# Kernel optimization log

Measured on AMD Instinct MI355X. Metric: run time of the kernel, lower is better.

Reference implementation:

```python
import jax, jax.numpy as jnp
import numpy as np

VOCAB = 32000
D_MODEL = 192
N_LAYERS = 8
D_STATE = 64
EXPAND = 2
D_CONV = 3
NUM_CLASSES = 2
D_INNER = EXPAND * D_MODEL            # 384
DT_RANK = (D_MODEL + 15) // 16        # 12 (mamba_ssm default ceil(d_model/16))
EPS = 1e-6


def rmsnorm(x, w):
    return w * x * jax.lax.rsqrt(jnp.mean(x * x, axis=-1, keepdims=True) + EPS)


def selective_scan(u, dt, A, Bm, Cm):
    # u, dt: (b, T, d_inner); Bm, Cm: (b, T, d_state); A: (d_inner, d_state)
    def step(h, xs):
        dt_t, B_t, C_t, u_t = xs                      # (b,di),(b,ds),(b,ds),(b,di)
        dA = jnp.exp(dt_t[:, :, None] * A)            # (b, di, ds)
        h = dA * h + (dt_t * u_t)[:, :, None] * B_t[:, None, :]
        y = jnp.einsum('bdn,bn->bd', h, C_t)
        return h, y

    b = u.shape[0]
    h0 = jnp.zeros((b, D_INNER, D_STATE), u.dtype)
    xs = (jnp.swapaxes(dt, 0, 1), jnp.swapaxes(Bm, 0, 1),
          jnp.swapaxes(Cm, 0, 1), jnp.swapaxes(u, 0, 1))
    _, ys = jax.lax.scan(step, h0, xs)                # ys: (T, b, di)
    return jnp.swapaxes(ys, 0, 1)


def mamba_layer(x, p):
    # one residual Mamba block: x + Mamba(RMSNorm(x))
    norm_w, in_w, cw, cb, xpw, dtw, dtb, Alog, Dp, ow = p
    h = rmsnorm(x, norm_w)
    xz = jnp.einsum('btd,ed->bte', h, in_w)           # (b, T, 2*di)
    xi, z = jnp.split(xz, 2, axis=-1)
    # causal depthwise conv over time
    xc = jnp.swapaxes(xi, 1, 2)                       # (b, di, T)
    xc = jax.lax.conv_general_dilated(xc, cw[:, None, :], (1,),
                                      [(D_CONV - 1, 0)],
                                      feature_group_count=D_INNER)
    xi = jax.nn.silu(jnp.swapaxes(xc, 1, 2) + cb)
    dbl = jnp.einsum('btc,ec->bte', xi, xpw)          # (b, T, dt_rank+2*ds)
    dt_r = dbl[..., :DT_RANK]
    Bm = dbl[..., DT_RANK:DT_RANK + D_STATE]
    Cm = dbl[..., DT_RANK + D_STATE:]
    dt = jax.nn.softplus(jnp.einsum('btr,dr->btd', dt_r, dtw) + dtb)
    A = -jnp.exp(Alog)
    y = selective_scan(xi, dt, A, Bm, Cm) + xi * Dp
    y = y * jax.nn.silu(z)
    return x + jnp.einsum('bte,de->btd', y, ow)


def setup_inputs():
    key = jax.random.key(0)
    ks = jax.random.split(key, 12)
    B, L = 8, 1024
    s = 0.02
    input_ids = jax.random.randint(ks[0], (B, L), 0, VOCAB, dtype=jnp.int32)
    attention_mask = jnp.ones((B, L), dtype=jnp.int32)
    embed = jax.random.normal(ks[1], (VOCAB, D_MODEL), jnp.float32) * s
    cls = jax.random.normal(ks[2], (1, 1, D_MODEL), jnp.float32) * s
    norm_w = jnp.ones((N_LAYERS, D_MODEL), jnp.float32)
    in_proj_w = jax.random.normal(ks[3], (N_LAYERS, 2 * D_INNER, D_MODEL), jnp.float32) * s
    conv_w = jax.random.normal(ks[4], (N_LAYERS, D_INNER, D_CONV), jnp.float32) * s
    conv_b = jnp.zeros((N_LAYERS, D_INNER), jnp.float32)
    x_proj_w = jax.random.normal(ks[5], (N_LAYERS, DT_RANK + 2 * D_STATE, D_INNER), jnp.float32) * s
    dt_proj_w = jax.random.normal(ks[6], (N_LAYERS, D_INNER, DT_RANK), jnp.float32) * s
    dt_proj_b = jnp.zeros((N_LAYERS, D_INNER), jnp.float32)
    # mamba_ssm S4D-real init: A_log = log(1..d_state)
    A_log = jnp.log(jnp.tile(jnp.arange(1.0, D_STATE + 1, dtype=jnp.float32)[None, None, :],
                             (N_LAYERS, D_INNER, 1)))
    D_param = jnp.ones((N_LAYERS, D_INNER), jnp.float32)
    out_proj_w = jax.random.normal(ks[7], (N_LAYERS, D_MODEL, D_INNER), jnp.float32) * s
    final_norm_w = jnp.ones((D_MODEL,), jnp.float32)
    head_w = embed[:NUM_CLASSES]            # tie_embeddings=True
    head_b = jnp.zeros((NUM_CLASSES,), jnp.float32)
    return dict(input_ids=input_ids, attention_mask=attention_mask, embed=embed,
                cls=cls, norm_w=norm_w, in_proj_w=in_proj_w, conv_w=conv_w,
                conv_b=conv_b, x_proj_w=x_proj_w, dt_proj_w=dt_proj_w,
                dt_proj_b=dt_proj_b, A_log=A_log, D_param=D_param,
                out_proj_w=out_proj_w, final_norm_w=final_norm_w,
                head_w=head_w, head_b=head_b)


def reference(input_ids, attention_mask, embed, cls, norm_w, in_proj_w, conv_w,
              conv_b, x_proj_w, dt_proj_w, dt_proj_b, A_log, D_param,
              out_proj_w, final_norm_w, head_w, head_b):
    x = embed[input_ids]                               # (b, L, d)
    b = x.shape[0]
    x = jnp.concatenate([x, jnp.broadcast_to(cls, (b, 1, D_MODEL))], axis=1)
    layer_fn = jax.checkpoint(mamba_layer)

    def body(x, p):
        return layer_fn(x, p), None

    x, _ = jax.lax.scan(body, x, (norm_w, in_proj_w, conv_w, conv_b, x_proj_w,
                                  dt_proj_w, dt_proj_b, A_log, D_param, out_proj_w))
    x = rmsnorm(x, final_norm_w)
    m = attention_mask.astype(x.dtype)                 # (b, L)
    denom = jnp.clip(jnp.sum(m, axis=1, keepdims=True), 1.0, None)
    pooled = jnp.sum(x[:, :-1] * m[..., None], axis=1) / denom
    return pooled @ head_w.T + head_b                  # (b, num_classes)
```

## Files before the change

### kernel.cpp

```cpp
#include <hip/hip_runtime.h>
#include <hip/hip_bf16.h>
#include <cstddef>

namespace {

constexpr int NB   = 8;
constexpr int LSEQ = 1025;
constexpr int TSEQ = 1024;
constexpr int DM   = 192;
constexpr int DI   = 384;
constexpr int DXZ  = 768;
constexpr int DBLW = 140;
constexpr int DTR  = 12;
constexpr int NST  = 64;
constexpr int MROWS = NB * LSEQ;
constexpr int NCH  = 64;
constexpr int CS   = 16;
constexpr int NCH1 = NCH - 1;
constexpr int NDG  = DI / 64;
constexpr int HST  = 32;
constexpr int XPAD = 144;
constexpr float LOG2E = 1.4426950408889634f;

using bf16x8 = __attribute__((ext_vector_type(8))) short;
using f32x4  = __attribute__((ext_vector_type(4))) float;

__device__ __forceinline__ float waveReduceSum(float v) {
#pragma unroll
  for (int o = 32; o; o >>= 1) v += __shfl_xor(v, o, 64);
  return v;
}

__device__ __forceinline__ unsigned short f2bf(float v) {
  __hip_bfloat16 b = __float2bfloat16(v);
  return *reinterpret_cast<unsigned short*>(&b);
}
__device__ __forceinline__ float bf2f(unsigned short u) {
  return __uint_as_float(((unsigned)u) << 16);
}
__device__ __forceinline__ unsigned addpair_bf(unsigned a, unsigned b) {
  float alo = __uint_as_float(a << 16), ahi = __uint_as_float(a & 0xffff0000u);
  float blo = __uint_as_float(b << 16), bhi = __uint_as_float(b & 0xffff0000u);
  return ((unsigned)f2bf(alo + blo)) | (((unsigned)f2bf(ahi + bhi)) << 16);
}

__global__ void embed_kernel(const int* __restrict__ ids, const float* __restrict__ emb,
                             const float* __restrict__ cls, float* __restrict__ x) {
  int idx = blockIdx.x * blockDim.x + threadIdx.x;
  if (idx >= NB * LSEQ * DM) return;
  int d = idx % DM;
  int bt = idx / DM;
  int t = bt % LSEQ, b = bt / LSEQ;
  float v;
  if (t < TSEQ) v = emb[(size_t)ids[b * TSEQ + t] * DM + d];
  else          v = cls[d];
  x[idx] = v;
}

__global__ void cvt_bf16_kernel(const float* __restrict__ src, unsigned short* __restrict__ dst,
                                int n) {
  int idx = blockIdx.x * blockDim.x + threadIdx.x;
  if (idx < n) dst[idx] = f2bf(src[idx]);
}

__global__ void pad_xp_kernel(const float* __restrict__ src, unsigned short* __restrict__ dst) {
  int idx = blockIdx.x * blockDim.x + threadIdx.x;
  if (idx >= 8 * XPAD * DI) return;
  int k = idx % DI;
  int n = (idx / DI) % XPAD;
  int l = idx / (DI * XPAD);
  float v = (n < DBLW) ? src[((size_t)l * DBLW + n) * DI + k] : 0.f;
  dst[idx] = f2bf(v);
}

__global__ void transpose_batched(const float* __restrict__ in, float* __restrict__ out,
                                  int rows, int cols) {
  __shared__ float tile[32][33];
  int l = blockIdx.z;
  int r0 = blockIdx.y * 32, c0 = blockIdx.x * 32;
  const float* src = in + (size_t)l * rows * cols;
  float* dst = out + (size_t)l * rows * cols;
  int tx = threadIdx.x, ty = threadIdx.y;
#pragma unroll
  for (int i = 0; i < 32; i += 8) {
    int r = r0 + ty + i, c = c0 + tx;
    if (r < rows && c < cols) tile[ty + i][tx] = src[(size_t)r * cols + c];
  }
  __syncthreads();
#pragma unroll
  for (int i = 0; i < 32; i += 8) {
    int c = c0 + ty + i, r = r0 + tx;
    if (c < cols && r < rows) dst[(size_t)c * rows + r] = tile[tx][ty + i];
  }
}

__global__ __launch_bounds__(192)
void rmsnorm_kernel(const float* __restrict__ x, const float* __restrict__ w,
                    unsigned short* __restrict__ h) {
  int row = blockIdx.x;
  int d = threadIdx.x;
  float v = x[(size_t)row * DM + d];
  float ss = waveReduceSum(v * v);
  __shared__ float red[3];
  if ((d & 63) == 0) red[d >> 6] = ss;
  __syncthreads();
  float ms = (red[0] + red[1] + red[2]) * (1.f / DM);
  h[(size_t)row * DM + d] = f2bf(v * rsqrtf(ms + 1e-6f) * w[d]);
}

template <int EPI, int ASRC>
__global__ __launch_bounds__(256)
void gemm_mfma(const unsigned short* __restrict__ A, const unsigned short* __restrict__ Ab0,
               const unsigned short* __restrict__ Ab1, const unsigned short* __restrict__ W,
               float* __restrict__ C, unsigned short* __restrict__ Cb,
               int M, int Nw, int Nstore, int K, int ldc) {
  __shared__ unsigned short Alds[128][40];
  __shared__ unsigned short Wlds[64][40];
  const int tid = threadIdx.x;
  const int w = tid >> 6, lane = tid & 63;
  const int r16 = lane & 15, g = lane >> 4;
  const int row0 = blockIdx.y * 128, col0 = blockIdx.x * 64;

  f32x4 acc[2][4];
#pragma unroll
  for (int mi = 0; mi < 2; ++mi)
#pragma unroll
    for (int ni = 0; ni < 4; ++ni) acc[mi][ni] = (f32x4){0.f, 0.f, 0.f, 0.f};

  for (int k0 = 0; k0 < K; k0 += 32) {
#pragma unroll
    for (int cc = 0; cc < 2; ++cc) {
      int c = tid + cc * 256;
      int r = c >> 2, q = c & 3;
      uint4 v = make_uint4(0, 0, 0, 0);
      int grow = row0 + r;
      if (grow < M) {
        if (ASRC == 0) {
          v = *(const uint4*)(A + (size_t)grow * K + k0 + q * 8);
        } else {
          uint4 a = *(const uint4*)(Ab0 + (size_t)grow * K + k0 + q * 8);
          uint4 b = *(const uint4*)(Ab1 + (size_t)grow * K + k0 + q * 8);
          v.x = addpair_bf(a.x, b.x);
          v.y = addpair_bf(a.y, b.y);
          v.z = addpair_bf(a.z, b.z);
          v.w = addpair_bf(a.w, b.w);
        }
      }
      *(uint4*)&Alds[r][q * 8] = v;
    }
    {
      int r = tid >> 2, q = tid & 3;
      uint4 v = make_uint4(0, 0, 0, 0);
      int gn = col0 + r;
      if (gn < Nw) v = *(const uint4*)(W + (size_t)gn * K + k0 + q * 8);
      *(uint4*)&Wlds[r][q * 8] = v;
    }
    __syncthreads();
    bf16x8 a_f[2], b_f[4];
#pragma unroll
    for (int mi = 0; mi < 2; ++mi)
      a_f[mi] = *(const bf16x8*)&Alds[w * 32 + mi * 16 + r16][g * 8];
#pragma unroll
    for (int ni = 0; ni < 4; ++ni)
      b_f[ni] = *(const bf16x8*)&Wlds[ni * 16 + r16][g * 8];
#pragma unroll
    for (int mi = 0; mi < 2; ++mi)
#pragma unroll
      for (int ni = 0; ni < 4; ++ni)
        acc[mi][ni] = __builtin_amdgcn_mfma_f32_16x16x32_bf16(a_f[mi], b_f[ni],
                                                              acc[mi][ni], 0, 0, 0);
    __syncthreads();
  }
#pragma unroll
  for (int mi = 0; mi < 2; ++mi) {
#pragma unroll
    for (int reg = 0; reg < 4; ++reg) {
      int row = row0 + w * 32 + mi * 16 + g * 4 + reg;
      if (row >= M) continue;
#pragma unroll
      for (int ni = 0; ni < 4; ++ni) {
        int col = col0 + ni * 16 + r16;
        if (col >= Nstore) continue;
        size_t idx = (size_t)row * ldc + col;
        if (EPI == 1)      C[idx] += acc[mi][ni][reg];
        else if (EPI == 0) C[idx] = acc[mi][ni][reg];
        else               Cb[idx] = f2bf(acc[mi][ni][reg]);
      }
    }
  }
}

__global__ void conv_kernel(const unsigned short* __restrict__ xz16, const float* __restrict__ cw,
                            const float* __restrict__ cb,
                            unsigned short* __restrict__ xi16,
                            unsigned short* __restrict__ zg16) {
  int idx = blockIdx.x * blockDim.x + threadIdx.x;
  if (idx >= NB * LSEQ * DI) return;
  int c = idx % DI;
  int bt = idx / DI;
  int t = bt % LSEQ, b = bt / LSEQ;
  const unsigned short* src = xz16 + (size_t)b * LSEQ * DXZ + c;
  float s = cb[c];
  float w0 = cw[c * 3 + 0], w1 = cw[c * 3 + 1], w2 = cw[c * 3 + 2];
  if (t >= 2) s = fmaf(w0, bf2f(src[(size_t)(t - 2) * DXZ]), s);
  if (t >= 1) s = fmaf(w1, bf2f(src[(size_t)(t - 1) * DXZ]), s);
  s = fmaf(w2, bf2f(src[(size_t)t * DXZ]), s);
  float sig = 1.f / (1.f + __expf(-s));
  float u = s * sig;
  xi16[idx] = f2bf(u);
  float zv = bf2f(src[(size_t)t * DXZ + DI]);
  float zsig = 1.f / (1.f + __expf(-zv));
  zg16[idx] = f2bf(zv * zsig);
}

__global__ __launch_bounds__(384)
void dt_kernel(const float* __restrict__ dbl, const float* __restrict__ dtwT,
               const float* __restrict__ dtb, float* __restrict__ dtout) {
  int row0 = blockIdx.x * 4;
  int d = threadIdx.x;
  __shared__ float rr[4][DTR];
  if (d < 4 * DTR) rr[d / DTR][d % DTR] = dbl[(size_t)(row0 + d / DTR) * DBLW + (d % DTR)];
  float w[DTR];
#pragma unroll
  for (int r = 0; r < DTR; ++r) w[r] = dtwT[r * DI + d];
  float bias = dtb[d];
  __syncthreads();
#pragma unroll
  for (int q = 0; q < 4; ++q) {
    float s = bias;
#pragma unroll
    for (int r = 0; r < DTR; ++r) s = fmaf(rr[q][r], w[r], s);
    float sp = fmaxf(s, 0.f) + log1pf(__expf(-fabsf(s)));
    dtout[(size_t)(row0 + q) * DI + d] = sp;
  }
}


__global__ __launch_bounds__(768, 6)
void scan_pass1(const float* __restrict__ dtp_, const unsigned short* __restrict__ xi16,
                const float* __restrict__ dbl, const float* __restrict__ Alog,
                float* __restrict__ cumdt, float* __restrict__ H) {
  __shared__ float Bt[CS][64];
  const int tid = threadIdx.x;
  const int w = tid >> 6, lane = tid & 63;
  const int dgrp = w >> 1, half = w & 1;
  const int b = blockIdx.x / NCH1;
  const int c = blockIdx.x % NCH1;
  const int bg = b * NDG + dgrp;
  const int d = dgrp * 64 + lane;
  const int n0 = half * HST;
  const int t0 = c * CS;

  {
    const float* srcB = dbl + ((size_t)b * LSEQ + t0) * DBLW + DTR + lane;
    for (int r = w; r < CS; r += 12) Bt[r][lane] = srcB[(size_t)r * DBLW];
  }

  const float* Ap = Alog + (size_t)d * NST;
  float a0 = __expf(Ap[0]);
  bool okl = true;
#pragma unroll
  for (int j = 0; j < HST; ++j) {
    float aj = __expf(Ap[n0 + j]);
    okl = okl && (fabsf(aj - (float)(n0 + j + 1) * a0) <= 1e-3f * (float)(n0 + j + 1) * fabsf(a0));
  }
  const bool fast = __all(okl);
  const float al2u = -a0 * LOG2E;

  float h[HST];
#pragma unroll
  for (int j = 0; j < HST; ++j) h[j] = 0.f;

  __syncthreads();

  const float* dtp = dtp_ + ((size_t)b * LSEQ + t0) * DI + d;
  const unsigned short* up = xi16 + ((size_t)b * LSEQ + t0) * DI + d;
  float cum = 0.f;
  float dtv = *dtp, uv = bf2f(*up);

  if (fast) {
    for (int t = 0; t < CS; ++t) {
      float n_dt = 0.f, n_u = 0.f;
      if (t + 1 < CS) {
        dtp += DI; up += DI;
        n_dt = *dtp; n_u = bf2f(*up);
      }
      float dtu = dtv * uv;
      float m = dtv * al2u;
      float r1 = exp2f(m);
      float p = (n0 == 0) ? r1 : exp2f(m * (float)(n0 + 1));
      float r2 = r1 * r1, r4 = r2 * r2;
      float s0 = p, s1 = p * r1, s2 = p * r2, s3 = s2 * r1;
#pragma unroll
      for (int k = 0; k < 8; ++k) {
        float4 B4 = *(const float4*)&Bt[t][n0 + 4 * k];
        h[4 * k + 0] = fmaf(s0, h[4 * k + 0], dtu * B4.x);
        h[4 * k + 1] = fmaf(s1, h[4 * k + 1], dtu * B4.y);
        h[4 * k + 2] = fmaf(s2, h[4 * k + 2], dtu * B4.z);
        h[4 * k + 3] = fmaf(s3, h[4 * k + 3], dtu * B4.w);
        if (k < 7) { s0 *= r4; s1 *= r4; s2 *= r4; s3 *= r4; }
      }
      cum += dtv;
      dtv = n_dt; uv = n_u;
    }
  } else {
    for (int t = 0; t < CS; ++t) {
      float n_dt = 0.f, n_u = 0.f;
      if (t + 1 < CS) {
        dtp += DI; up += DI;
        n_dt = *dtp; n_u = bf2f(*up);
      }
      float dtu = dtv * uv;
      for (int j = 0; j < HST; ++j) {
        float aj = -__expf(Ap[n0 + j]) * LOG2E;
        h[j] = fmaf(exp2f(dtv * aj), h[j], dtu * Bt[t][n0 + j]);
      }
      cum += dtv;
      dtv = n_dt; uv = n_u;
    }
  }

  if (half == 0)
    cumdt[(size_t)bg * NCH1 * 64 + (size_t)c * 64 + lane] = cum;
  float* hp = H + ((size_t)bg * NCH + (c + 1)) * NST * 64 + (size_t)n0 * 64 + lane;
#pragma unroll
  for (int j = 0; j < HST; ++j) hp[j * 64] = h[j];
}

__global__ __launch_bounds__(256)
void scan_pass2(const float* __restrict__ cumdt, const float* __restrict__ Alog,
                float* __restrict__ H) {
  int gw = blockIdx.x * 4 + (threadIdx.x >> 6);
  int lane = threadIdx.x & 63;
  int bg = gw >> 4;
  int nq = (gw & 15) * 4;
  int dgrp = bg % NDG;
  int d = dgrp * 64 + lane;

  float al2[4];
#pragma unroll
  for (int j = 0; j < 4; ++j) al2[j] = -__expf(Alog[(size_t)d * NST + nq + j]) * LOG2E;

  float h[4] = {0.f, 0.f, 0.f, 0.f};

  float* H0 = H + ((size_t)bg * NCH) * NST * 64 + (size_t)nq * 64 + lane;
#pragma unroll
  for (int j = 0; j < 4; ++j) H0[j * 64] = 0.f;

  for (int c = 1; c < NCH; ++c) {
    float cum = cumdt[(size_t)bg * NCH1 * 64 + (size_t)(c - 1) * 64 + lane];
    float* Hc = H + ((size_t)bg * NCH + c) * NST * 64 + (size_t)nq * 64 + lane;
#pragma unroll
    for (int j = 0; j < 4; ++j) {
      float he = Hc[j * 64];
      h[j] = fmaf(exp2f(al2[j] * cum), h[j], he);
      Hc[j * 64] = h[j];
    }
  }
}

__global__ __launch_bounds__(768, 6)
void scan_pass3(const float* __restrict__ dtp_, const unsigned short* __restrict__ xi16,
                const unsigned short* __restrict__ zg16, const float* __restrict__ dbl,
                const float* __restrict__ Alog, const float* __restrict__ Dpar,
                const float* __restrict__ H, unsigned short* __restrict__ yb0,
                unsigned short* __restrict__ yb1) {
  __shared__ float Bt[CS + 1][64];
  __shared__ float Ct[CS + 1][64];
  const int tid = threadIdx.x;
  const int w = tid >> 6, lane = tid & 63;
  const int dgrp = w >> 1, half = w & 1;
  const int b = blockIdx.x >> 6;
  const int c = blockIdx.x & 63;
  const int bg = b * NDG + dgrp;
  const int d = dgrp * 64 + lane;
  const int n0 = half * HST;
  const int t0 = c * CS;
  const int nsteps = (c == NCH - 1) ? (LSEQ - t0) : CS;

  {
    if (w < 6) {
      const float* srcB = dbl + ((size_t)b * LSEQ + t0) * DBLW + DTR + lane;
      for (int r = w; r < nsteps; r += 6) Bt[r][lane] = srcB[(size_t)r * DBLW];
    } else {
      const float* srcC = dbl + ((size_t)b * LSEQ + t0) * DBLW + DTR + NST + lane;
      for (int r = w - 6; r < nsteps; r += 6) Ct[r][lane] = srcC[(size_t)r * DBLW];
    }
  }

  const float* Ap = Alog + (size_t)d * NST;
  float a0 = __expf(Ap[0]);
  bool okl = true;
#pragma unroll
  for (int j = 0; j < HST; ++j) {
    float aj = __expf(Ap[n0 + j]);
    okl = okl && (fabsf(aj - (float)(n0 + j + 1) * a0) <= 1e-3f * (float)(n0 + j + 1) * fabsf(a0));
  }
  const bool fast = __all(okl);
  const float al2u = -a0 * LOG2E;

  float Dp = Dpar[d];
  float h[HST];
  {
    const float* hi = H + ((size_t)bg * NCH + c) * NST * 64 + (size_t)n0 * 64 + lane;
#pragma unroll
    for (int j = 0; j < HST; ++j) h[j] = hi[j * 64];
  }

  __syncthreads();

  const float* dtp = dtp_ + ((size_t)b * LSEQ + t0) * DI + d;
  const unsigned short* up = xi16 + ((size_t)b * LSEQ + t0) * DI + d;
  const unsigned short* gp = zg16 + ((size_t)b * LSEQ + t0) * DI + d;
  unsigned short* yp = (half == 0 ? yb0 : yb1) + ((size_t)b * LSEQ + t0) * DI + d;

  float dtv = *dtp, uv = bf2f(*up), gv = bf2f(*gp);

  if (fast) {
    for (int t = 0; t < nsteps; ++t) {
      float n_dt = 0.f, n_u = 0.f, n_g = 0.f;
      if (t + 1 < nsteps) {
        dtp += DI; up += DI; gp += DI;
        n_dt = *dtp; n_u = bf2f(*up); n_g = bf2f(*gp);
      }
      float dtu = dtv * uv;
      float m = dtv * al2u;
      float r1 = exp2f(m);
      float p = (n0 == 0) ? r1 : exp2f(m * (float)(n0 + 1));
      float r2 = r1 * r1, r4 = r2 * r2;
      float s0 = p, s1 = p * r1, s2 = p * r2, s3 = s2 * r1;
      float y = 0.f;
#pragma unroll
      for (int k = 0; k < 8; ++k) {
        float4 B4 = *(const float4*)&Bt[t][n0 + 4 * k];
        float4 C4 = *(const float4*)&Ct[t][n0 + 4 * k];
        h[4 * k + 0] = fmaf(s0, h[4 * k + 0], dtu * B4.x);
        y = fmaf(h[4 * k + 0], C4.x, y);
        h[4 * k + 1] = fmaf(s1, h[4 * k + 1], dtu * B4.y);
        y = fmaf(h[4 * k + 1], C4.y, y);
        h[4 * k + 2] = fmaf(s2, h[4 * k + 2], dtu * B4.z);
        y = fmaf(h[4 * k + 2], C4.z, y);
        h[4 * k + 3] = fmaf(s3, h[4 * k + 3], dtu * B4.w);
        y = fmaf(h[4 * k + 3], C4.w, y);
        if (k < 7) { s0 *= r4; s1 *= r4; s2 *= r4; s3 *= r4; }
      }
      float outv = (half == 0) ? fmaf(uv, Dp, y) * gv : y * gv;
      *yp = f2bf(outv);
      yp += DI;
      dtv = n_dt; uv = n_u; gv = n_g;
    }
  } else {
    for (int t = 0; t < nsteps; ++t) {
      float n_dt = 0.f, n_u = 0.f, n_g = 0.f;
      if (t + 1 < nsteps) {
        dtp += DI; up += DI; gp += DI;
        n_dt = *dtp; n_u = bf2f(*up); n_g = bf2f(*gp);
      }
      float dtu = dtv * uv;
      float y = 0.f;
      for (int j = 0; j < HST; ++j) {
        float aj = -__expf(Ap[n0 + j]) * LOG2E;
        h[j] = fmaf(exp2f(dtv * aj), h[j], dtu * Bt[t][n0 + j]);
        y = fmaf(h[j], Ct[t][n0 + j], y);
      }
      float outv = (half == 0) ? fmaf(uv, Dp, y) * gv : y * gv;
      *yp = f2bf(outv);
      yp += DI;
      dtv = n_dt; uv = n_u; gv = n_g;
    }
  }
}

__global__ __launch_bounds__(192)
void pool1_kernel(const float* __restrict__ x, const int* __restrict__ mask,
                  const float* __restrict__ fw, float* __restrict__ partial) {
  int b = blockIdx.x >> 6;
  int chunk = blockIdx.x & 63;
  int d = threadIdx.x;
  __shared__ float red[3];
  float w = fw[d];
  float acc = 0.f;
  for (int tt = 0; tt < 16; ++tt) {
    int t = chunk * 16 + tt;
    float v = x[((size_t)b * LSEQ + t) * DM + d];
    float ss = waveReduceSum(v * v);
    if ((d & 63) == 0) red[d >> 6] = ss;
    __syncthreads();
    float ms = (red[0] + red[1] + red[2]) * (1.f / DM);
    float m = (float)mask[b * TSEQ + t];
    acc = fmaf(v * rsqrtf(ms + 1e-6f) * w, m, acc);
    __syncthreads();
  }
  partial[((size_t)b * 64 + chunk) * DM + d] = acc;
}

__global__ __launch_bounds__(192)
void pool2_kernel(const float* __restrict__ partial, const int* __restrict__ mask,
                  const float* __restrict__ hw, const float* __restrict__ hb,
                  float* __restrict__ out) {
  int b = blockIdx.x;
  int d = threadIdx.x;
  float s = 0.f;
  for (int c = 0; c < 64; ++c) s += partial[((size_t)b * 64 + c) * DM + d];
  float den = 0.f;
  for (int t = d; t < TSEQ; t += DM) den += (float)mask[b * TSEQ + t];
  den = waveReduceSum(den);
  __shared__ float dred[3];
  __shared__ float pooled[DM];
  if ((d & 63) == 0) dred[d >> 6] = den;
  __syncthreads();
  float denom = fmaxf(dred[0] + dred[1] + dred[2], 1.f);
  pooled[d] = s / denom;
  __syncthreads();
  if (d < 2) {
    float acc = hb[d];
    for (int k = 0; k < DM; ++k) acc = fmaf(pooled[k], hw[d * DM + k], acc);
    out[b * 2 + d] = acc;
  }
}

}

extern "C" void kernel_launch(void* const* d_in, const int* in_sizes, int n_in,
                              void* d_out, int out_size, void* d_ws, size_t ws_size,
                              hipStream_t stream) {
  const int*   ids    = (const int*)d_in[0];
  const int*   mask   = (const int*)d_in[1];
  const float* embed  = (const float*)d_in[2];
  const float* cls    = (const float*)d_in[3];
  const float* norm_w = (const float*)d_in[4];
  const float* in_w   = (const float*)d_in[5];
  const float* conv_w = (const float*)d_in[6];
  const float* conv_b = (const float*)d_in[7];
  const float* xp_w   = (const float*)d_in[8];
  const float* dtw    = (const float*)d_in[9];
  const float* dtb    = (const float*)d_in[10];
  const float* Alog   = (const float*)d_in[11];
  const float* Dpar   = (const float*)d_in[12];
  const float* ow     = (const float*)d_in[13];
  const float* fnw    = (const float*)d_in[14];
  const float* hw     = (const float*)d_in[15];
  const float* hb     = (const float*)d_in[16];
  float* out = (float*)d_out;

  char* base = (char*)d_ws;
  size_t off = 0;
  auto alloc = [&](size_t bytes) -> void* {
    void* p = base + off;
    off = (off + bytes + 255) & ~(size_t)255;
    return p;
  };

  float* x      = (float*)alloc((size_t)NB * LSEQ * DM * 4);
  unsigned short* h16 = (unsigned short*)alloc((size_t)NB * LSEQ * DM * 2);
  unsigned short* xz16 = (unsigned short*)alloc((size_t)NB * LSEQ * DXZ * 2);
  unsigned short* xi16 = (unsigned short*)alloc((size_t)NB * LSEQ * DI * 2);
  unsigned short* zg16 = (unsigned short*)alloc((size_t)NB * LSEQ * DI * 2);
  float* dblb   = (float*)alloc((size_t)NB * LSEQ * DBLW * 4);
  float* dtbuf  = (float*)alloc((size_t)NB * LSEQ * DI * 4);
  unsigned short* yb0 = (unsigned short*)alloc((size_t)NB * LSEQ * DI * 2);
  unsigned short* yb1 = (unsigned short*)alloc((size_t)NB * LSEQ * DI * 2);
  unsigned short* wb_in = (unsigned short*)alloc((size_t)8 * DXZ * DM * 2);
  unsigned short* wb_xp = (unsigned short*)alloc((size_t)8 * XPAD * DI * 2);
  unsigned short* wb_ow = (unsigned short*)alloc((size_t)8 * DM * DI * 2);
  float* wT_dt  = (float*)alloc((size_t)8 * DTR * DI * 4);
  float* partial = (float*)alloc((size_t)NB * 64 * DM * 4);
  float* cumdt  = (float*)alloc((size_t)NB * NDG * NCH1 * 64 * 4);
  float* Hbuf   = (float*)alloc((size_t)NB * NDG * NCH * NST * 64 * 4);

  cvt_bf16_kernel<<<(8 * DXZ * DM + 255) / 256, 256, 0, stream>>>(in_w, wb_in, 8 * DXZ * DM);
  pad_xp_kernel<<<(8 * XPAD * DI + 255) / 256, 256, 0, stream>>>(xp_w, wb_xp);
  cvt_bf16_kernel<<<(8 * DM * DI + 255) / 256, 256, 0, stream>>>(ow, wb_ow, 8 * DM * DI);
  dim3 tb(32, 8);
  transpose_batched<<<dim3(1, 12, 8), tb, 0, stream>>>(dtw, wT_dt, DI, DTR);

  embed_kernel<<<(NB * LSEQ * DM) / 256, 256, 0, stream>>>(ids, embed, cls, x);

  const int mtiles = (MROWS + 127) / 128;
  for (int l = 0; l < 8; ++l) {
    rmsnorm_kernel<<<MROWS, 192, 0, stream>>>(x, norm_w + l * DM, h16);
    gemm_mfma<2, 0><<<dim3(DXZ / 64, mtiles), 256, 0, stream>>>(
        h16, nullptr, nullptr, wb_in + (size_t)l * DXZ * DM, nullptr, xz16,
        MROWS, DXZ, DXZ, DM, DXZ);
    conv_kernel<<<(NB * LSEQ * DI) / 256, 256, 0, stream>>>(
        xz16, conv_w + l * DI * 3, conv_b + l * DI, xi16, zg16);
    gemm_mfma<0, 0><<<dim3(XPAD / 64 + 1, mtiles), 256, 0, stream>>>(
        xi16, nullptr, nullptr, wb_xp + (size_t)l * XPAD * DI, dblb, nullptr,
        MROWS, XPAD, DBLW, DI, DBLW);
    dt_kernel<<<MROWS / 4, DI, 0, stream>>>(dblb, wT_dt + l * DTR * DI, dtb + l * DI, dtbuf);
    scan_pass1<<<NB * NCH1, 768, 0, stream>>>(
        dtbuf, xi16, dblb, Alog + (size_t)l * DI * NST, cumdt, Hbuf);
    scan_pass2<<<(NB * NDG * 16) / 4, 256, 0, stream>>>(
        cumdt, Alog + (size_t)l * DI * NST, Hbuf);
    scan_pass3<<<NB * NCH, 768, 0, stream>>>(
        dtbuf, xi16, zg16, dblb, Alog + (size_t)l * DI * NST, Dpar + l * DI, Hbuf,
        yb0, yb1);
    gemm_mfma<1, 1><<<dim3(DM / 64, mtiles), 256, 0, stream>>>(
        nullptr, yb0, yb1, wb_ow + (size_t)l * DM * DI, x, nullptr,
        MROWS, DM, DM, DI, DM);
  }

  pool1_kernel<<<NB * 64, 192, 0, stream>>>(x, mask, fnw, partial);
  pool2_kernel<<<NB, 192, 0, stream>>>(partial, mask, hw, hb, out);
}
```

Baseline: 1.391 ms.

## Fuse RMSNorm into in-proj GEMM, halve scan chunks, store chunk states in bf16

Folds the RMSNorm into the input-projection GEMM: each block computes per-row inverse RMS from fp32 x and converts normalized values to bf16 while filling LDS, removing the separate norm kernel and the h16 buffer round trip. The chunked scan now uses 32 chunks of 32 steps instead of 64 of 16, and inter-chunk states are stored as bf16, cutting H traffic while lowering occupancy hints. The scan output dot product is split into four accumulators for ILP. Risks include bf16 precision loss in the carried states, recomputation of the row norms in every column tile, and fewer blocks in the scan passes.

```diff
diff --git a/kernel.cpp b/kernel.cpp
--- a/kernel.cpp
+++ b/kernel.cpp
@@ -14,8 +14,8 @@
 constexpr int DTR  = 12;
 constexpr int NST  = 64;
 constexpr int MROWS = NB * LSEQ;
-constexpr int NCH  = 64;
-constexpr int CS   = 16;
+constexpr int NCH  = 32;
+constexpr int CS   = 32;
 constexpr int NCH1 = NCH - 1;
 constexpr int NDG  = DI / 64;
 constexpr int HST  = 32;
@@ -94,26 +94,103 @@
   }
 }
 
-__global__ __launch_bounds__(192)
-void rmsnorm_kernel(const float* __restrict__ x, const float* __restrict__ w,
-                    unsigned short* __restrict__ h) {
-  int row = blockIdx.x;
-  int d = threadIdx.x;
-  float v = x[(size_t)row * DM + d];
-  float ss = waveReduceSum(v * v);
-  __shared__ float red[3];
-  if ((d & 63) == 0) red[d >> 6] = ss;
+__global__ __launch_bounds__(256)
+void gemm_in_fused(const float* __restrict__ X, const float* __restrict__ normw,
+                   const unsigned short* __restrict__ W, unsigned short* __restrict__ Cb,
+                   int M) {
+  __shared__ unsigned short Alds[128][40];
+  __shared__ unsigned short Wlds[64][40];
+  __shared__ float invr[128];
+  __shared__ float nw[DM];
+  const int tid = threadIdx.x;
+  const int w = tid >> 6, lane = tid & 63;
+  const int r16 = lane & 15, g = lane >> 4;
+  const int row0 = blockIdx.y * 128, col0 = blockIdx.x * 64;
+
+  if (tid < DM) nw[tid] = normw[tid];
+  {
+    int r = tid >> 1, u = tid & 1;
+    int grow = row0 + r;
+    float ss = 0.f;
+    if (grow < M) {
+      const float4* src = (const float4*)(X + (size_t)grow * DM + u * 96);
+#pragma unroll
+      for (int i = 0; i < 24; ++i) {
+        float4 v = src[i];
+        ss += v.x * v.x + v.y * v.y + v.z * v.z + v.w * v.w;
+      }
+    }
+    ss += __shfl_xor(ss, 1, 64);
+    if (u == 0) invr[r] = rsqrtf(ss * (1.f / DM) + 1e-6f);
+  }
   __syncthreads();
-  float ms = (red[0] + red[1] + red[2]) * (1.f / DM);
-  h[(size_t)row * DM + d] = f2bf(v * rsqrtf(ms + 1e-6f) * w[d]);
+
+  f32x4 acc[2][4];
+#pragma unroll
+  for (int mi = 0; mi < 2; ++mi)
+#pragma unroll
+    for (int ni = 0; ni < 4; ++ni) acc[mi][ni] = (f32x4){0.f, 0.f, 0.f, 0.f};
+
+  for (int k0 = 0; k0 < DM; k0 += 32) {
+#pragma unroll
+    for (int cc = 0; cc < 2; ++cc) {
+      int c = tid + cc * 256;
+      int r = c >> 2, q = c & 3;
+      uint4 v = make_uint4(0, 0, 0, 0);
+      int grow = row0 + r;
+      if (grow < M) {
+        const float* s0 = X + (size_t)grow * DM + k0 + q * 8;
+        float4 p0 = *(const float4*)s0, p1 = *(const float4*)(s0 + 4);
+        float ir = invr[r];
+        int kk = k0 + q * 8;
+        v.x = (unsigned)f2bf(p0.x * ir * nw[kk + 0]) | ((unsigned)f2bf(p0.y * ir * nw[kk + 1]) << 16);
+        v.y = (unsigned)f2bf(p0.z * ir * nw[kk + 2]) | ((unsigned)f2bf(p0.w * ir * nw[kk + 3]) << 16);
+        v.z = (unsigned)f2bf(p1.x * ir * nw[kk + 4]) | ((unsigned)f2bf(p1.y * ir * nw[kk + 5]) << 16);
+        v.w = (unsigned)f2bf(p1.z * ir * nw[kk + 6]) | ((unsigned)f2bf(p1.w * ir * nw[kk + 7]) << 16);
+      }
+      *(uint4*)&Alds[r][q * 8] = v;
+    }
+    {
+      int r = tid >> 2, q = tid & 3;
+      uint4 v = *(const uint4*)(W + (size_t)(col0 + r) * DM + k0 + q * 8);
+      *(uint4*)&Wlds[r][q * 8] = v;
+    }
+    __syncthreads();
+    bf16x8 a_f[2], b_f[4];
+#pragma unroll
+    for (int mi = 0; mi < 2; ++mi)
+      a_f[mi] = *(const bf16x8*)&Alds[w * 32 + mi * 16 + r16][g * 8];
+#pragma unroll
+    for (int ni = 0; ni < 4; ++ni)
+      b_f[ni] = *(const bf16x8*)&Wlds[ni * 16 + r16][g * 8];
+#pragma unroll
+    for (int mi = 0; mi < 2; ++mi)
+#pragma unroll
+      for (int ni = 0; ni < 4; ++ni)
+        acc[mi][ni] = __builtin_amdgcn_mfma_f32_16x16x32_bf16(a_f[mi], b_f[ni],
+                                                              acc[mi][ni], 0, 0, 0);
+    __syncthreads();
+  }
+#pragma unroll
+  for (int mi = 0; mi < 2; ++mi) {
+#pragma unroll
+    for (int reg = 0; reg < 4; ++reg) {
+      int row = row0 + w * 32 + mi * 16 + g * 4 + reg;
+      if (row >= M) continue;
+#pragma unroll
+      for (int ni = 0; ni < 4; ++ni) {
+        int col = col0 + ni * 16 + r16;
+        Cb[(size_t)row * DXZ + col] = f2bf(acc[mi][ni][reg]);
+      }
+    }
+  }
 }
 
 template <int EPI, int ASRC>
 __global__ __launch_bounds__(256)
 void gemm_mfma(const unsigned short* __restrict__ A, const unsigned short* __restrict__ Ab0,
                const unsigned short* __restrict__ Ab1, const unsigned short* __restrict__ W,
-               float* __restrict__ C, unsigned short* __restrict__ Cb,
-               int M, int Nw, int Nstore, int K, int ldc) {
+               float* __restrict__ C, int M, int Nw, int Nstore, int K, int ldc) {
   __shared__ unsigned short Alds[128][40];
   __shared__ unsigned short Wlds[64][40];
   const int tid = threadIdx.x;
@@ -182,9 +259,8 @@
         int col = col0 + ni * 16 + r16;
         if (col >= Nstore) continue;
         size_t idx = (size_t)row * ldc + col;
-        if (EPI == 1)      C[idx] += acc[mi][ni][reg];
-        else if (EPI == 0) C[idx] = acc[mi][ni][reg];
-        else               Cb[idx] = f2bf(acc[mi][ni][reg]);
+        if (EPI == 1) C[idx] += acc[mi][ni][reg];
+        else          C[idx] = acc[mi][ni][reg];
       }
     }
   }
@@ -236,10 +312,10 @@
 }
 
 
-__global__ __launch_bounds__(768, 6)
+__global__ __launch_bounds__(768, 3)
 void scan_pass1(const float* __restrict__ dtp_, const unsigned short* __restrict__ xi16,
                 const float* __restrict__ dbl, const float* __restrict__ Alog,
-                float* __restrict__ cumdt, float* __restrict__ H) {
+                float* __restrict__ cumdt, unsigned short* __restrict__ H) {
   __shared__ float Bt[CS][64];
   const int tid = threadIdx.x;
   const int w = tid >> 6, lane = tid & 63;
@@ -322,14 +398,14 @@
 
   if (half == 0)
     cumdt[(size_t)bg * NCH1 * 64 + (size_t)c * 64 + lane] = cum;
-  float* hp = H + ((size_t)bg * NCH + (c + 1)) * NST * 64 + (size_t)n0 * 64 + lane;
-#pragma unroll
-  for (int j = 0; j < HST; ++j) hp[j * 64] = h[j];
+  unsigned short* hp = H + ((size_t)bg * NCH + (c + 1)) * NST * 64 + (size_t)n0 * 64 + lane;
+#pragma unroll
+  for (int j = 0; j < HST; ++j) hp[j * 64] = f2bf(h[j]);
 }
 
 __global__ __launch_bounds__(256)
 void scan_pass2(const float* __restrict__ cumdt, const float* __restrict__ Alog,
-                float* __restrict__ H) {
+                unsigned short* __restrict__ H) {
   int gw = blockIdx.x * 4 + (threadIdx.x >> 6);
   int lane = threadIdx.x & 63;
   int bg = gw >> 4;
@@ -343,35 +419,35 @@
 
   float h[4] = {0.f, 0.f, 0.f, 0.f};
 
-  float* H0 = H + ((size_t)bg * NCH) * NST * 64 + (size_t)nq * 64 + lane;
-#pragma unroll
-  for (int j = 0; j < 4; ++j) H0[j * 64] = 0.f;
+  unsigned short* H0 = H + ((size_t)bg * NCH) * NST * 64 + (size_t)nq * 64 + lane;
+#pragma unroll
+  for (int j = 0; j < 4; ++j) H0[j * 64] = 0;
 
   for (int c = 1; c < NCH; ++c) {
     float cum = cumdt[(size_t)bg * NCH1 * 64 + (size_t)(c - 1) * 64 + lane];
-    float* Hc = H + ((size_t)bg * NCH + c) * NST * 64 + (size_t)nq * 64 + lane;
+    unsigned short* Hc = H + ((size_t)bg * NCH + c) * NST * 64 + (size_t)nq * 64 + lane;
 #pragma unroll
     for (int j = 0; j < 4; ++j) {
-      float he = Hc[j * 64];
+      float he = bf2f(Hc[j * 64]);
       h[j] = fmaf(exp2f(al2[j] * cum), h[j], he);
-      Hc[j * 64] = h[j];
-    }
-  }
-}
-
-__global__ __launch_bounds__(768, 6)
+      Hc[j * 64] = f2bf(h[j]);
+    }
+  }
+}
+
+__global__ __launch_bounds__(768, 3)
 void scan_pass3(const float* __restrict__ dtp_, const unsigned short* __restrict__ xi16,
                 const unsigned short* __restrict__ zg16, const float* __restrict__ dbl,
                 const float* __restrict__ Alog, const float* __restrict__ Dpar,
-                const float* __restrict__ H, unsigned short* __restrict__ yb0,
+                const unsigned short* __restrict__ H, unsigned short* __restrict__ yb0,
                 unsigned short* __restrict__ yb1) {
   __shared__ float Bt[CS + 1][64];
   __shared__ float Ct[CS + 1][64];
   const int tid = threadIdx.x;
   const int w = tid >> 6, lane = tid & 63;
   const int dgrp = w >> 1, half = w & 1;
-  const int b = blockIdx.x >> 6;
-  const int c = blockIdx.x & 63;
+  const int b = blockIdx.x >> 5;
+  const int c = blockIdx.x & 31;
   const int bg = b * NDG + dgrp;
   const int d = dgrp * 64 + lane;
   const int n0 = half * HST;
@@ -402,9 +478,9 @@
   float Dp = Dpar[d];
   float h[HST];
   {
-    const float* hi = H + ((size_t)bg * NCH + c) * NST * 64 + (size_t)n0 * 64 + lane;
-#pragma unroll
-    for (int j = 0; j < HST; ++j) h[j] = hi[j * 64];
+    const unsigned short* hi = H + ((size_t)bg * NCH + c) * NST * 64 + (size_t)n0 * 64 + lane;
+#pragma unroll
+    for (int j = 0; j < HST; ++j) h[j] = bf2f(hi[j * 64]);
   }
 
   __syncthreads();
@@ -429,21 +505,22 @@
       float p = (n0 == 0) ? r1 : exp2f(m * (float)(n0 + 1));
       float r2 = r1 * r1, r4 = r2 * r2;
       float s0 = p, s1 = p * r1, s2 = p * r2, s3 = s2 * r1;
-      float y = 0.f;
+      float y0 = 0.f, y1 = 0.f, y2 = 0.f, y3 = 0.f;
 #pragma unroll
       for (int k = 0; k < 8; ++k) {
         float4 B4 = *(const float4*)&Bt[t][n0 + 4 * k];
         float4 C4 = *(const float4*)&Ct[t][n0 + 4 * k];
         h[4 * k + 0] = fmaf(s0, h[4 * k + 0], dtu * B4.x);
-        y = fmaf(h[4 * k + 0], C4.x, y);
+        y0 = fmaf(h[4 * k + 0], C4.x, y0);
         h[4 * k + 1] = fmaf(s1, h[4 * k + 1], dtu * B4.y);
-        y = fmaf(h[4 * k + 1], C4.y, y);
+        y1 = fmaf(h[4 * k + 1], C4.y, y1);
         h[4 * k + 2] = fmaf(s2, h[4 * k + 2], dtu * B4.z);
-        y = fmaf(h[4 * k + 2], C4.z, y);
+        y2 = fmaf(h[4 * k + 2], C4.z, y2);
         h[4 * k + 3] = fmaf(s3, h[4 * k + 3], dtu * B4.w);
-        y = fmaf(h[4 * k + 3], C4.w, y);
+        y3 = fmaf(h[4 * k + 3], C4.w, y3);
         if (k < 7) { s0 *= r4; s1 *= r4; s2 *= r4; s3 *= r4; }
       }
+      float y = (y0 + y1) + (y2 + y3);
       float outv = (half == 0) ? fmaf(uv, Dp, y) * gv : y * gv;
       *yp = f2bf(outv);
       yp += DI;
@@ -552,7 +629,6 @@
   };
 
   float* x      = (float*)alloc((size_t)NB * LSEQ * DM * 4);
-  unsigned short* h16 = (unsigned short*)alloc((size_t)NB * LSEQ * DM * 2);
   unsigned short* xz16 = (unsigned short*)alloc((size_t)NB * LSEQ * DXZ * 2);
   unsigned short* xi16 = (unsigned short*)alloc((size_t)NB * LSEQ * DI * 2);
   unsigned short* zg16 = (unsigned short*)alloc((size_t)NB * LSEQ * DI * 2);
@@ -566,7 +642,7 @@
   float* wT_dt  = (float*)alloc((size_t)8 * DTR * DI * 4);
   float* partial = (float*)alloc((size_t)NB * 64 * DM * 4);
   float* cumdt  = (float*)alloc((size_t)NB * NDG * NCH1 * 64 * 4);
-  float* Hbuf   = (float*)alloc((size_t)NB * NDG * NCH * NST * 64 * 4);
+  unsigned short* Hbuf = (unsigned short*)alloc((size_t)NB * NDG * NCH * NST * 64 * 2);
 
   cvt_bf16_kernel<<<(8 * DXZ * DM + 255) / 256, 256, 0, stream>>>(in_w, wb_in, 8 * DXZ * DM);
   pad_xp_kernel<<<(8 * XPAD * DI + 255) / 256, 256, 0, stream>>>(xp_w, wb_xp);
@@ -578,14 +654,12 @@
 
   const int mtiles = (MROWS + 127) / 128;
   for (int l = 0; l < 8; ++l) {
-    rmsnorm_kernel<<<MROWS, 192, 0, stream>>>(x, norm_w + l * DM, h16);
-    gemm_mfma<2, 0><<<dim3(DXZ / 64, mtiles), 256, 0, stream>>>(
-        h16, nullptr, nullptr, wb_in + (size_t)l * DXZ * DM, nullptr, xz16,
-        MROWS, DXZ, DXZ, DM, DXZ);
+    gemm_in_fused<<<dim3(DXZ / 64, mtiles), 256, 0, stream>>>(
+        x, norm_w + l * DM, wb_in + (size_t)l * DXZ * DM, xz16, MROWS);
     conv_kernel<<<(NB * LSEQ * DI) / 256, 256, 0, stream>>>(
         xz16, conv_w + l * DI * 3, conv_b + l * DI, xi16, zg16);
     gemm_mfma<0, 0><<<dim3(XPAD / 64 + 1, mtiles), 256, 0, stream>>>(
-        xi16, nullptr, nullptr, wb_xp + (size_t)l * XPAD * DI, dblb, nullptr,
+        xi16, nullptr, nullptr, wb_xp + (size_t)l * XPAD * DI, dblb,
         MROWS, XPAD, DBLW, DI, DBLW);
     dt_kernel<<<MROWS / 4, DI, 0, stream>>>(dblb, wT_dt + l * DTR * DI, dtb + l * DI, dtbuf);
     scan_pass1<<<NB * NCH1, 768, 0, stream>>>(
@@ -596,7 +670,7 @@
         dtbuf, xi16, zg16, dblb, Alog + (size_t)l * DI * NST, Dpar + l * DI, Hbuf,
         yb0, yb1);
     gemm_mfma<1, 1><<<dim3(DM / 64, mtiles), 256, 0, stream>>>(
-        nullptr, yb0, yb1, wb_ow + (size_t)l * DM * DI, x, nullptr,
+        nullptr, yb0, yb1, wb_ow + (size_t)l * DM * DI, x,
         MROWS, DM, DM, DI, DM);
   }
 
```

After: 1.343 ms. 1.04x faster.
